# Optimization experiments

Hardware: AMD Instinct MI355X
Metric: run time of the kernel (lower is better)

The kernel has to match this reference:

```python
import jax, jax.numpy as jnp
import numpy as np

N_INPUTS = 1024
N_MIDDLE = 256
N_OUTPUTS = 64
BATCH = 65536


def setup_inputs() -> dict:
    key = jax.random.key(0)
    k_x, k_w1, k_w2 = jax.random.split(key, 3)
    x = jax.random.normal(k_x, (BATCH, N_INPUTS), dtype=jnp.float32)
    # Synapse weights k are initialized with random.random() in [0, 1)
    W1 = jax.random.uniform(k_w1, (N_MIDDLE, N_INPUTS), dtype=jnp.float32)
    W2 = jax.random.uniform(k_w2, (N_OUTPUTS, N_MIDDLE), dtype=jnp.float32)
    # Neuron biases b are initialized to 0.0
    b1 = jnp.zeros((N_MIDDLE,), dtype=jnp.float32)
    b2 = jnp.zeros((N_OUTPUTS,), dtype=jnp.float32)
    return {"x": x, "W1": W1, "b1": b1, "W2": W2, "b2": b2}


def reference(x, W1, b1, W2, b2):
    # Middle RegularNeurons: relu(sum_j k_ij * x_j + b_i)
    h = jax.nn.relu(jnp.einsum('bi,mi->bm', x, W1) + b1)  # [B, n_middle]
    # Output DestinationNeurons: relu(sum_m k_om * h_m + b_o)
    y = jax.nn.relu(jnp.einsum('bm,om->bo', h, W2) + b2)  # [B, n_outputs]
    return y
```

## Files before the change

kernel.cpp:

```cpp
#include <hip/hip_runtime.h>
#include <stdint.h>

#define NIN 1024
#define NMID 256
#define NOUT 64

typedef __attribute__((ext_vector_type(8))) short bf16x8;
typedef __attribute__((ext_vector_type(4))) float fx4;

union FragU { bf16x8 v; uint32_t u[4]; };

__device__ __forceinline__ uint32_t cvtpk(float lo, float hi) {
  uint32_t r;
  asm("v_cvt_pk_bf16_f32 %0, %1, %2" : "=v"(r) : "v"(lo), "v"(hi));
  return r;
}

__device__ __forceinline__ void gload16(const void* g, void* l) {
  __builtin_amdgcn_global_load_lds(
      (const __attribute__((address_space(1))) uint32_t*)g,
      (__attribute__((address_space(3))) uint32_t*)l, 16, 0, 0);
}

__global__ __launch_bounds__(256) void cvt_weights(
    const float* __restrict__ W1, const float* __restrict__ W2,
    unsigned short* __restrict__ w1b, unsigned short* __restrict__ w2b) {
  int i = blockIdx.x * 256 + threadIdx.x;
  int e = i << 2;
  const int n1 = NMID * NIN;
  if (e < n1) {
    fx4 v = *(const fx4*)(W1 + e);
    uint2 p;
    p.x = cvtpk(v.x, v.y);
    p.y = cvtpk(v.z, v.w);
    *(uint2*)(w1b + e) = p;
  } else {
    int e2 = e - n1;
    if (e2 < NOUT * NMID) {
      fx4 v = *(const fx4*)(W2 + e2);
      uint2 p;
      p.x = cvtpk(v.x, v.y);
      p.y = cvtpk(v.z, v.w);
      *(uint2*)(w2b + e2) = p;
    }
  }
}

__global__ __launch_bounds__(256) void livenet_main(
    const float* __restrict__ x,
    const unsigned short* __restrict__ w1b,
    const float* __restrict__ b1,
    const unsigned short* __restrict__ w2b,
    const float* __restrict__ b2,
    float* __restrict__ y) {

  __shared__ __align__(16) char smem[49152];

  const int tid = threadIdx.x;
  const int lane = tid & 63;
  const int wn = tid >> 6;
  const int l15 = lane & 15;
  const int lg = lane >> 4;
  const int row0 = blockIdx.x * 64;

  uint32_t xoff[4];
#pragma unroll
  for (int i = 0; i < 4; ++i) {
    uint32_t o = (uint32_t)(i * 4096 + tid * 16);
    uint32_t r = o >> 8;
    uint32_t pc = (o >> 4) & 15u;
    uint32_t j = pc ^ (r & 15u);
    xoff[i] = (uint32_t)(row0 + (int)r) * NIN + j * 4u;
  }
  uint32_t woff[8];
#pragma unroll
  for (int i = 0; i < 8; ++i) {
    uint32_t o = (uint32_t)(i * 4096 + tid * 16);
    uint32_t r = o >> 7;
    uint32_t pc = (o >> 4) & 7u;
    uint32_t j = pc ^ (r & 7u);
    woff[i] = r * NIN + j * 8u;
  }

  fx4 acc[4][4];
#pragma unroll
  for (int i = 0; i < 4; ++i)
#pragma unroll
    for (int j = 0; j < 4; ++j)
      acc[i][j] = (fx4){0.f, 0.f, 0.f, 0.f};

  for (int ks = 0; ks < 16; ++ks) {
    const int k0 = ks * 64;
#pragma unroll
    for (int i = 0; i < 4; ++i)
      gload16(x + xoff[i] + k0, smem + i * 4096 + tid * 16);
#pragma unroll
    for (int i = 0; i < 8; ++i)
      gload16(w1b + woff[i] + k0, smem + 16384 + i * 4096 + tid * 16);
    __syncthreads();

    bf16x8 a[4][2], b[4][2];
#pragma unroll
    for (int i = 0; i < 4; ++i) {
      const char* rowp = smem + (16 * i + l15) * 256;
#pragma unroll
      for (int kk = 0; kk < 2; ++kk) {
        uint32_t j = kk * 8 + lg * 2;
        fx4 va = *(const fx4*)(rowp + (uint32_t)((j ^ (uint32_t)l15) << 4));
        fx4 vb = *(const fx4*)(rowp + (uint32_t)(((j + 1) ^ (uint32_t)l15) << 4));
        FragU f;
        f.u[0] = cvtpk(va.x, va.y);
        f.u[1] = cvtpk(va.z, va.w);
        f.u[2] = cvtpk(vb.x, vb.y);
        f.u[3] = cvtpk(vb.z, vb.w);
        a[i][kk] = f.v;
      }
    }
#pragma unroll
    for (int jn = 0; jn < 4; ++jn) {
      uint32_t rowN = (uint32_t)(wn * 64 + jn * 16 + l15);
      const char* rowp = smem + 16384 + rowN * 128;
#pragma unroll
      for (int kk = 0; kk < 2; ++kk) {
        uint32_t j = (uint32_t)(kk * 4 + lg);
        b[jn][kk] = *(const bf16x8*)(rowp + ((j ^ (rowN & 7u)) << 4));
      }
    }
#pragma unroll
    for (int i = 0; i < 4; ++i)
#pragma unroll
      for (int jn = 0; jn < 4; ++jn)
#pragma unroll
        for (int kk = 0; kk < 2; ++kk)
          acc[i][jn] = __builtin_amdgcn_mfma_f32_16x16x32_bf16(
              a[i][kk], b[jn][kk], acc[i][jn], 0, 0, 0);
    __syncthreads();
  }

  unsigned short* hs = (unsigned short*)smem;
  float bias1[4];
#pragma unroll
  for (int jn = 0; jn < 4; ++jn) bias1[jn] = b1[wn * 64 + jn * 16 + l15];

#pragma unroll
  for (int i = 0; i < 4; ++i) {
#pragma unroll
    for (int jn = 0; jn < 4; ++jn) {
      int col = wn * 64 + jn * 16 + l15;
#pragma unroll
      for (int rg = 0; rg < 4; ++rg) {
        float v = acc[i][jn][rg] + bias1[jn];
        v = v > 0.f ? v : 0.f;
        int row = i * 16 + lg * 4 + rg;
        hs[row * 264 + col] = (unsigned short)cvtpk(v, v);
      }
    }
  }
  __syncthreads();

  fx4 acc2[4];
#pragma unroll
  for (int jn = 0; jn < 4; ++jn) acc2[jn] = (fx4){0.f, 0.f, 0.f, 0.f};

#pragma unroll
  for (int ksb = 0; ksb < 8; ++ksb) {
    bf16x8 a2 = *(const bf16x8*)(hs + (wn * 16 + l15) * 264 + ksb * 32 + lg * 8);
#pragma unroll
    for (int jn = 0; jn < 4; ++jn) {
      bf16x8 bw = *(const bf16x8*)(w2b + (jn * 16 + l15) * NMID + ksb * 32 + lg * 8);
      acc2[jn] = __builtin_amdgcn_mfma_f32_16x16x32_bf16(a2, bw, acc2[jn], 0, 0, 0);
    }
  }

  float bias2[4];
#pragma unroll
  for (int jn = 0; jn < 4; ++jn) bias2[jn] = b2[jn * 16 + l15];

#pragma unroll
  for (int jn = 0; jn < 4; ++jn) {
#pragma unroll
    for (int rg = 0; rg < 4; ++rg) {
      float v = acc2[jn][rg] + bias2[jn];
      v = v > 0.f ? v : 0.f;
      int row = row0 + wn * 16 + lg * 4 + rg;
      y[(size_t)row * NOUT + jn * 16 + l15] = v;
    }
  }
}

extern "C" void kernel_launch(void* const* d_in, const int* in_sizes, int n_in,
                              void* d_out, int out_size, void* d_ws, size_t ws_size,
                              hipStream_t stream) {
  const float* x  = (const float*)d_in[0];
  const float* W1 = (const float*)d_in[1];
  const float* b1 = (const float*)d_in[2];
  const float* W2 = (const float*)d_in[3];
  const float* b2 = (const float*)d_in[4];
  float* y = (float*)d_out;

  unsigned short* w1b = (unsigned short*)d_ws;
  unsigned short* w2b = w1b + (size_t)NMID * NIN;

  const int batch = in_sizes[0] / NIN;

  const int tot4 = (NMID * NIN + NOUT * NMID) / 4;
  hipLaunchKernelGGL(cvt_weights, dim3((tot4 + 255) / 256), dim3(256), 0, stream,
                     W1, W2, w1b, w2b);
  hipLaunchKernelGGL(livenet_main, dim3(batch / 64), dim3(256), 0, stream,
                     x, w1b, b1, w2b, b2, y);
}
```

Before: 87.41 us.

## Double-buffer K loop, convert x once to bf16, use 32x32 MFMA on 128-row tiles

Raises the block tile to 128 rows with 8 waves and double-buffers LDS so the next x and W1 slices load while the current MFMAs run. x is read into registers, converted to bf16 once and written swizzled into LDS, instead of staging fp32 and converting per fragment. It also switches to 32x32x16 MFMAs and reworks the second GEMM onto them. The cost is 96KB of dynamic LDS per block, which limits occupancy, plus more register pressure from the larger accumulators.

```diff
diff --git a/kernel.cpp b/kernel.cpp
--- a/kernel.cpp
+++ b/kernel.cpp
@@ -4,11 +4,19 @@
 #define NIN 1024
 #define NMID 256
 #define NOUT 64
+#define BM 128
+#define BK 64
+#define NSTEP (NIN / BK)
 
 typedef __attribute__((ext_vector_type(8))) short bf16x8;
 typedef __attribute__((ext_vector_type(4))) float fx4;
-
-union FragU { bf16x8 v; uint32_t u[4]; };
+typedef __attribute__((ext_vector_type(16))) float f32x16;
+typedef __attribute__((ext_vector_type(4))) uint32_t u32x4;
+
+#define XS_TILE 16384
+#define W1_OFF  32768
+#define W1_TILE 32768
+#define LDS_SZ  98304
 
 __device__ __forceinline__ uint32_t cvtpk(float lo, float hi) {
   uint32_t r;
@@ -25,8 +33,7 @@
 __global__ __launch_bounds__(256) void cvt_weights(
     const float* __restrict__ W1, const float* __restrict__ W2,
     unsigned short* __restrict__ w1b, unsigned short* __restrict__ w2b) {
-  int i = blockIdx.x * 256 + threadIdx.x;
-  int e = i << 2;
+  int e = (blockIdx.x * 256 + threadIdx.x) << 2;
   const int n1 = NMID * NIN;
   if (e < n1) {
     fx4 v = *(const fx4*)(W1 + e);
@@ -46,7 +53,7 @@
   }
 }
 
-__global__ __launch_bounds__(256) void livenet_main(
+__global__ __launch_bounds__(512, 2) void livenet_main(
     const float* __restrict__ x,
     const unsigned short* __restrict__ w1b,
     const float* __restrict__ b1,
@@ -54,137 +61,178 @@
     const float* __restrict__ b2,
     float* __restrict__ y) {
 
-  __shared__ __align__(16) char smem[49152];
+  extern __shared__ __align__(16) char smem[];
 
   const int tid = threadIdx.x;
   const int lane = tid & 63;
-  const int wn = tid >> 6;
-  const int l15 = lane & 15;
-  const int lg = lane >> 4;
-  const int row0 = blockIdx.x * 64;
-
-  uint32_t xoff[4];
+  const int w = tid >> 6;
+  const int wm = w >> 2;
+  const int wn = w & 3;
+  const int l31 = lane & 31;
+  const int lh = lane >> 5;
+  const int row0 = blockIdx.x * BM;
+
+  const int xr_row = tid >> 2;
+  const int xr_c = tid & 3;
+  const float* xbase = x + (size_t)(row0 + xr_row) * NIN + xr_c * 16;
+  const int xrx = xr_row & 7;
+  const uint32_t xd0 = (uint32_t)(xr_row * 128 + (((2 * xr_c) ^ xrx) << 4));
+  const uint32_t xd1 = (uint32_t)(xr_row * 128 + (((2 * xr_c + 1) ^ xrx) << 4));
+
+  uint32_t w1src[4], w1dst[4];
 #pragma unroll
   for (int i = 0; i < 4; ++i) {
-    uint32_t o = (uint32_t)(i * 4096 + tid * 16);
-    uint32_t r = o >> 8;
-    uint32_t pc = (o >> 4) & 15u;
-    uint32_t j = pc ^ (r & 15u);
-    xoff[i] = (uint32_t)(row0 + (int)r) * NIN + j * 4u;
-  }
-  uint32_t woff[8];
-#pragma unroll
-  for (int i = 0; i < 8; ++i) {
-    uint32_t o = (uint32_t)(i * 4096 + tid * 16);
+    uint32_t o = (uint32_t)(i * 8192 + tid * 16);
     uint32_t r = o >> 7;
     uint32_t pc = (o >> 4) & 7u;
     uint32_t j = pc ^ (r & 7u);
-    woff[i] = r * NIN + j * 8u;
-  }
-
-  fx4 acc[4][4];
-#pragma unroll
-  for (int i = 0; i < 4; ++i)
-#pragma unroll
-    for (int j = 0; j < 4; ++j)
-      acc[i][j] = (fx4){0.f, 0.f, 0.f, 0.f};
-
-  for (int ks = 0; ks < 16; ++ks) {
-    const int k0 = ks * 64;
-#pragma unroll
-    for (int i = 0; i < 4; ++i)
-      gload16(x + xoff[i] + k0, smem + i * 4096 + tid * 16);
-#pragma unroll
-    for (int i = 0; i < 8; ++i)
-      gload16(w1b + woff[i] + k0, smem + 16384 + i * 4096 + tid * 16);
+    w1src[i] = r * NIN + j * 8u;
+    w1dst[i] = o;
+  }
+
+  fx4 xl[4];
+#define XLOAD(k0)                                     \
+  {                                                   \
+    const float* p_ = xbase + (k0);                   \
+    xl[0] = *(const fx4*)p_;                          \
+    xl[1] = *(const fx4*)(p_ + 4);                    \
+    xl[2] = *(const fx4*)(p_ + 8);                    \
+    xl[3] = *(const fx4*)(p_ + 12);                   \
+  }
+
+#define XWRITE(buf)                                                   \
+  {                                                                   \
+    u32x4 A_ = {cvtpk(xl[0].x, xl[0].y), cvtpk(xl[0].z, xl[0].w),     \
+                cvtpk(xl[1].x, xl[1].y), cvtpk(xl[1].z, xl[1].w)};    \
+    u32x4 B_ = {cvtpk(xl[2].x, xl[2].y), cvtpk(xl[2].z, xl[2].w),     \
+                cvtpk(xl[3].x, xl[3].y), cvtpk(xl[3].z, xl[3].w)};    \
+    char* xb_ = smem + (buf) * XS_TILE;                               \
+    *(u32x4*)(xb_ + xd0) = A_;                                        \
+    *(u32x4*)(xb_ + xd1) = B_;                                        \
+  }
+
+#define W1STAGE(buf, k0)                                                      \
+  {                                                                           \
+    char* wb_ = smem + W1_OFF + (buf) * W1_TILE;                              \
+    _Pragma("unroll") for (int i_ = 0; i_ < 4; ++i_)                          \
+        gload16(w1b + w1src[i_] + (k0), wb_ + w1dst[i_]);                     \
+  }
+
+  f32x16 acc[2][2];
+#pragma unroll
+  for (int mt = 0; mt < 2; ++mt)
+#pragma unroll
+    for (int nt = 0; nt < 2; ++nt)
+#pragma unroll
+      for (int q = 0; q < 16; ++q) acc[mt][nt][q] = 0.f;
+
+  W1STAGE(0, 0);
+  XLOAD(0);
+  XWRITE(0);
+  __syncthreads();
+
+  uint32_t aoff[2], boff[2];
+#pragma unroll
+  for (int mt = 0; mt < 2; ++mt) {
+    uint32_t R = (uint32_t)(wm * 64 + mt * 32 + l31);
+    aoff[mt] = R * 128u;
+  }
+#pragma unroll
+  for (int nt = 0; nt < 2; ++nt) {
+    uint32_t R = (uint32_t)(wn * 64 + nt * 32 + l31);
+    boff[nt] = R * 128u;
+  }
+  const uint32_t arx0 = (uint32_t)((wm * 64 + l31) & 7);
+  const uint32_t brx0 = (uint32_t)((wn * 64 + l31) & 7);
+
+  for (int ks = 0; ks < NSTEP; ++ks) {
+    const int cur = ks & 1, nxt = cur ^ 1;
+    if (ks + 1 < NSTEP) {
+      W1STAGE(nxt, (ks + 1) * BK);
+      XLOAD((ks + 1) * BK);
+    }
+
+    char* xsb = smem + cur * XS_TILE;
+    char* w1sb = smem + W1_OFF + cur * W1_TILE;
+
+    bf16x8 a[2][4], b[2][4];
+#pragma unroll
+    for (int mt = 0; mt < 2; ++mt) {
+      uint32_t rx = arx0;
+#pragma unroll
+      for (int kk = 0; kk < 4; ++kk)
+        a[mt][kk] = *(const bf16x8*)(xsb + aoff[mt] +
+                                     ((((uint32_t)(kk * 2 + lh)) ^ rx) << 4));
+    }
+#pragma unroll
+    for (int nt = 0; nt < 2; ++nt) {
+      uint32_t rx = brx0;
+#pragma unroll
+      for (int kk = 0; kk < 4; ++kk)
+        b[nt][kk] = *(const bf16x8*)(w1sb + boff[nt] +
+                                     ((((uint32_t)(kk * 2 + lh)) ^ rx) << 4));
+    }
+
+#pragma unroll
+    for (int mt = 0; mt < 2; ++mt)
+#pragma unroll
+      for (int nt = 0; nt < 2; ++nt)
+#pragma unroll
+        for (int kk = 0; kk < 4; ++kk)
+          acc[mt][nt] = __builtin_amdgcn_mfma_f32_32x32x16_bf16(
+              a[mt][kk], b[nt][kk], acc[mt][nt], 0, 0, 0);
+
+    if (ks + 1 < NSTEP) XWRITE(nxt);
     __syncthreads();
-
-    bf16x8 a[4][2], b[4][2];
-#pragma unroll
-    for (int i = 0; i < 4; ++i) {
-      const char* rowp = smem + (16 * i + l15) * 256;
-#pragma unroll
-      for (int kk = 0; kk < 2; ++kk) {
-        uint32_t j = kk * 8 + lg * 2;
-        fx4 va = *(const fx4*)(rowp + (uint32_t)((j ^ (uint32_t)l15) << 4));
-        fx4 vb = *(const fx4*)(rowp + (uint32_t)(((j + 1) ^ (uint32_t)l15) << 4));
-        FragU f;
-        f.u[0] = cvtpk(va.x, va.y);
-        f.u[1] = cvtpk(va.z, va.w);
-        f.u[2] = cvtpk(vb.x, vb.y);
-        f.u[3] = cvtpk(vb.z, vb.w);
-        a[i][kk] = f.v;
+  }
+
+  float b1v[2];
+#pragma unroll
+  for (int nt = 0; nt < 2; ++nt) b1v[nt] = b1[wn * 64 + nt * 32 + l31];
+
+#pragma unroll
+  for (int mt = 0; mt < 2; ++mt) {
+#pragma unroll
+    for (int nt = 0; nt < 2; ++nt) {
+      int col = wn * 64 + nt * 32 + l31;
+#pragma unroll
+      for (int rg = 0; rg < 16; ++rg) {
+        int row = wm * 64 + mt * 32 + (rg & 3) + 8 * (rg >> 2) + 4 * lh;
+        float v = acc[mt][nt][rg] + b1v[nt];
+        v = v > 0.f ? v : 0.f;
+        int j = (col >> 3) ^ (row & 31);
+        *(unsigned short*)(smem + row * 512 + (j << 4) + (col & 7) * 2) =
+            (unsigned short)cvtpk(v, v);
       }
     }
-#pragma unroll
-    for (int jn = 0; jn < 4; ++jn) {
-      uint32_t rowN = (uint32_t)(wn * 64 + jn * 16 + l15);
-      const char* rowp = smem + 16384 + rowN * 128;
-#pragma unroll
-      for (int kk = 0; kk < 2; ++kk) {
-        uint32_t j = (uint32_t)(kk * 4 + lg);
-        b[jn][kk] = *(const bf16x8*)(rowp + ((j ^ (rowN & 7u)) << 4));
-      }
-    }
-#pragma unroll
-    for (int i = 0; i < 4; ++i)
-#pragma unroll
-      for (int jn = 0; jn < 4; ++jn)
-#pragma unroll
-        for (int kk = 0; kk < 2; ++kk)
-          acc[i][jn] = __builtin_amdgcn_mfma_f32_16x16x32_bf16(
-              a[i][kk], b[jn][kk], acc[i][jn], 0, 0, 0);
-    __syncthreads();
-  }
-
-  unsigned short* hs = (unsigned short*)smem;
-  float bias1[4];
-#pragma unroll
-  for (int jn = 0; jn < 4; ++jn) bias1[jn] = b1[wn * 64 + jn * 16 + l15];
-
-#pragma unroll
-  for (int i = 0; i < 4; ++i) {
-#pragma unroll
-    for (int jn = 0; jn < 4; ++jn) {
-      int col = wn * 64 + jn * 16 + l15;
-#pragma unroll
-      for (int rg = 0; rg < 4; ++rg) {
-        float v = acc[i][jn][rg] + bias1[jn];
-        v = v > 0.f ? v : 0.f;
-        int row = i * 16 + lg * 4 + rg;
-        hs[row * 264 + col] = (unsigned short)cvtpk(v, v);
-      }
-    }
   }
   __syncthreads();
 
-  fx4 acc2[4];
-#pragma unroll
-  for (int jn = 0; jn < 4; ++jn) acc2[jn] = (fx4){0.f, 0.f, 0.f, 0.f};
-
-#pragma unroll
-  for (int ksb = 0; ksb < 8; ++ksb) {
-    bf16x8 a2 = *(const bf16x8*)(hs + (wn * 16 + l15) * 264 + ksb * 32 + lg * 8);
-#pragma unroll
-    for (int jn = 0; jn < 4; ++jn) {
-      bf16x8 bw = *(const bf16x8*)(w2b + (jn * 16 + l15) * NMID + ksb * 32 + lg * 8);
-      acc2[jn] = __builtin_amdgcn_mfma_f32_16x16x32_bf16(a2, bw, acc2[jn], 0, 0, 0);
-    }
-  }
-
-  float bias2[4];
-#pragma unroll
-  for (int jn = 0; jn < 4; ++jn) bias2[jn] = b2[jn * 16 + l15];
-
-#pragma unroll
-  for (int jn = 0; jn < 4; ++jn) {
-#pragma unroll
-    for (int rg = 0; rg < 4; ++rg) {
-      float v = acc2[jn][rg] + bias2[jn];
-      v = v > 0.f ? v : 0.f;
-      int row = row0 + wn * 16 + lg * 4 + rg;
-      y[(size_t)row * NOUT + jn * 16 + l15] = v;
-    }
+  f32x16 acc2;
+#pragma unroll
+  for (int q = 0; q < 16; ++q) acc2[q] = 0.f;
+
+  const int r2 = (w >> 1) * 32;
+  const int c2 = (w & 1) * 32;
+  const int arow = r2 + l31;
+  const uint32_t arx = (uint32_t)(arow & 31);
+  const unsigned short* w2row = w2b + (size_t)(c2 + l31) * NMID + lh * 8;
+
+#pragma unroll
+  for (int kk = 0; kk < 16; ++kk) {
+    bf16x8 a2 = *(const bf16x8*)(smem + arow * 512 +
+                                 ((((uint32_t)(kk * 2 + lh)) ^ arx) << 4));
+    bf16x8 bw = *(const bf16x8*)(w2row + kk * 16);
+    acc2 = __builtin_amdgcn_mfma_f32_32x32x16_bf16(a2, bw, acc2, 0, 0, 0);
+  }
+
+  float bias2 = b2[c2 + l31];
+#pragma unroll
+  for (int rg = 0; rg < 16; ++rg) {
+    int row = r2 + (rg & 3) + 8 * (rg >> 2) + 4 * lh;
+    float v = acc2[rg] + bias2;
+    v = v > 0.f ? v : 0.f;
+    y[(size_t)(row0 + row) * NOUT + c2 + l31] = v;
   }
 }
 
@@ -206,6 +254,13 @@
   const int tot4 = (NMID * NIN + NOUT * NMID) / 4;
   hipLaunchKernelGGL(cvt_weights, dim3((tot4 + 255) / 256), dim3(256), 0, stream,
                      W1, W2, w1b, w2b);
-  hipLaunchKernelGGL(livenet_main, dim3(batch / 64), dim3(256), 0, stream,
+
+  static int lds_set = 0;
+  if (!lds_set) {
+    hipFuncSetAttribute((const void*)livenet_main,
+                        hipFuncAttributeMaxDynamicSharedMemorySize, LDS_SZ);
+    lds_set = 1;
+  }
+  hipLaunchKernelGGL(livenet_main, dim3(batch / BM), dim3(512), LDS_SZ, stream,
                      x, w1b, b1, w2b, b2, y);
 }
```

Measured after the change: 81.86 us. -6.3%, faster.
